# Kernel optimization log

Measured on AMD Instinct MI355X. Metric: run time of the kernel, lower is better.

Reference implementation:

```python
import jax, jax.numpy as jnp
import numpy as np

C = 128      # in channels
CO = 64      # out channels
G = 32       # group-norm groups
RES_IN = 32  # input resolution
RES_OUT = 64 # subdivided resolution
N = 20000    # active input voxels
EPS = 1e-5


def setup_inputs() -> dict:
    key = jax.random.key(0)
    ks = jax.random.split(key, 12)
    # unique active voxel coords at RES_IN (batch index 0, single instance)
    rng = np.random.default_rng(0)
    flat = rng.choice(RES_IN ** 3, size=N, replace=False)
    xyz = np.stack([flat // (RES_IN * RES_IN), (flat // RES_IN) % RES_IN, flat % RES_IN], axis=1)
    x_coords = jnp.asarray(np.concatenate([np.zeros((N, 1), np.int32), xyz.astype(np.int32)], axis=1))
    x_feats = jax.random.normal(ks[0], (N, C), dtype=jnp.float32)
    gn1_g = 1.0 + 0.1 * jax.random.normal(ks[1], (C,), dtype=jnp.float32)
    gn1_b = 0.1 * jax.random.normal(ks[2], (C,), dtype=jnp.float32)
    W1 = 0.05 * jax.random.normal(ks[3], (3, 3, 3, C, CO), dtype=jnp.float32)
    b1 = 0.01 * jax.random.normal(ks[4], (CO,), dtype=jnp.float32)
    gn2_g = 1.0 + 0.1 * jax.random.normal(ks[5], (CO,), dtype=jnp.float32)
    gn2_b = 0.1 * jax.random.normal(ks[6], (CO,), dtype=jnp.float32)
    W2 = 0.05 * jax.random.normal(ks[7], (3, 3, 3, CO, CO), dtype=jnp.float32)  # zero_module in source; random here to exercise math
    b2 = 0.01 * jax.random.normal(ks[8], (CO,), dtype=jnp.float32)
    Ws = 0.05 * jax.random.normal(ks[9], (C, CO), dtype=jnp.float32)   # 1x1 skip conv
    bs = 0.01 * jax.random.normal(ks[10], (CO,), dtype=jnp.float32)
    return dict(x_feats=x_feats, x_coords=x_coords, gn1_g=gn1_g, gn1_b=gn1_b,
                W1=W1, b1=b1, gn2_g=gn2_g, gn2_b=gn2_b, W2=W2, b2=b2, Ws=Ws, bs=bs)


def group_norm(f, g, b):
    # single-instance sparse group norm: stats per group over all points
    n, c = f.shape
    x = f.reshape(n, G, c // G)
    mu = jnp.mean(x, axis=(0, 2), keepdims=True)
    var = jnp.mean((x - mu) ** 2, axis=(0, 2), keepdims=True)
    return ((x - mu) * jax.lax.rsqrt(var + EPS)).reshape(n, c) * g + b


def subdivide(coords, feats):
    n = coords.shape[0]
    offs = jnp.stack(jnp.meshgrid(jnp.arange(2), jnp.arange(2), jnp.arange(2), indexing='ij'), -1).reshape(8, 3)
    xyz = coords[:, None, 1:] * 2 + offs[None].astype(coords.dtype)          # [n,8,3]
    bidx = jnp.broadcast_to(coords[:, None, :1], (n, 8, 1))
    new_coords = jnp.concatenate([bidx, xyz], axis=-1).reshape(n * 8, 4)
    return new_coords, jnp.repeat(feats, 8, axis=0)


def subm_conv3(coords, feats, W, b):
    # submanifold 3x3x3 sparse conv: scatter to padded dense grid, gather 27 neighbors per active site
    cin = feats.shape[1]
    grid = jnp.zeros((RES_OUT + 2, RES_OUT + 2, RES_OUT + 2, cin), feats.dtype)
    grid = grid.at[coords[:, 1] + 1, coords[:, 2] + 1, coords[:, 3] + 1].set(feats)
    acc = jnp.zeros((feats.shape[0], W.shape[-1]), feats.dtype)
    for i in range(3):
        for j in range(3):
            for k in range(3):
                nb = grid[coords[:, 1] + i, coords[:, 2] + j, coords[:, 3] + k]  # [n, cin]
                acc = acc + nb @ W[i, j, k]
    return acc + b


def reference(x_feats, x_coords, gn1_g, gn1_b, W1, b1, gn2_g, gn2_b, W2, b2, Ws, bs):
    h = jax.nn.silu(group_norm(x_feats, gn1_g, gn1_b))
    hc, hf = subdivide(x_coords, h)
    _, xf = subdivide(x_coords, x_feats)
    hf = subm_conv3(hc, hf, W1, b1)
    hf = jax.nn.silu(group_norm(hf, gn2_g, gn2_b))
    hf = subm_conv3(hc, hf, W2, b2)
    out = hf + (xf @ Ws + bs)  # residual + 1x1 skip conv (out_channels != channels)
    return out
```

## Files before the change

### kernel.cpp

```cpp
#include <hip/hip_runtime.h>
#include <hip/hip_bf16.h>
#include <math.h>

#define N_PTS 20000
#define C_IN 128
#define C_OUT 64
#define M_PTS (N_PTS*8)
#define EPS 1e-5f

typedef __attribute__((ext_vector_type(8))) short short8;
typedef __attribute__((ext_vector_type(4))) float float4v;

__device__ __forceinline__ ushort f2bf(float f){
    unsigned int i = __float_as_uint(f);
    unsigned int r = i + 0x7fffu + ((i >> 16) & 1u);
    return (ushort)(r >> 16);
}
__device__ __forceinline__ float bf2f(ushort u){ return __uint_as_float(((unsigned int)u) << 16); }
__device__ __forceinline__ float silu(float z){ return z / (1.f + expf(-z)); }
__device__ __forceinline__ int cmp5(int v){
    v &= 0x1249; v = (v | (v >> 2)) & 0x10C3; v = (v | (v >> 4)) & 0x100F; v = (v | (v >> 8)) & 0x1F;
    return v;
}


__global__ void __launch_bounds__(256) prep_kernel(
    const float* __restrict__ W1, const float* __restrict__ W2,
    ushort* __restrict__ Wt1, ushort* __restrict__ Wt2,
    int* __restrict__ pg, ushort* __restrict__ h, ushort* __restrict__ h2,
    const float* __restrict__ x, float* __restrict__ stats)
{
    const int b = blockIdx.x, tid = threadIdx.x;
    if (b < 2048){
        int idx = b * 256 + tid;
        int j = idx & 7, l = (idx >> 3) & 63, nb = (idx >> 9) & 3, kb = (idx >> 11) & 3, t = idx >> 13;
        int ci = kb * 32 + (l >> 4) * 8 + j, co = nb * 16 + (l & 15);
        int o = t >> 3, jj = t & 7;
        int ox = (o >> 2) & 1, oy = (o >> 1) & 1, oz = o & 1;
        int jx = (jj >> 2) & 1, jy = (jj >> 1) & 1, jz = jj & 1;
        float s = 0.f;
#pragma unroll
        for (int dx = -1; dx <= 1; dx++){
            if (((ox + dx) >> 1) != ox + jx - 1) continue;
#pragma unroll
            for (int dy = -1; dy <= 1; dy++){
                if (((oy + dy) >> 1) != oy + jy - 1) continue;
#pragma unroll
                for (int dz = -1; dz <= 1; dz++){
                    if (((oz + dz) >> 1) != oz + jz - 1) continue;
                    s += W1[((dx+1)*9 + (dy+1)*3 + (dz+1)) * (C_IN*64) + ci * 64 + co];
                }
            }
        }
        Wt1[idx] = f2bf(s);
    } else if (b < 2480){
        int idx = (b - 2048) * 256 + tid;
        int j = idx & 7, l = (idx >> 3) & 63, nb = (idx >> 9) & 3, kb = (idx >> 11) & 1, t = idx >> 12;
        int ci = kb * 32 + (l >> 4) * 8 + j, co = nb * 16 + (l & 15);
        Wt2[idx] = f2bf(W2[(t * C_OUT + ci) * 64 + co]);
    } else if (b < 2608){
        int i = (b - 2480) * 256 + tid;
        pg[i] = -1;
        if (b == 2480){
            if (tid < C_IN) h[(size_t)N_PTS * C_IN + tid] = 0;
            if (tid < 256){
                h2[(size_t)M_PTS * C_OUT + tid] = 0;
                h2[(size_t)M_PTS * C_OUT + 256 + tid] = 0;
            }
        }
    } else {
        __shared__ float ls[64];
        if (tid < 64) ls[tid] = 0.f;
        __syncthreads();
        const int g = tid & 31;
        const int r0 = (b - 2608) * 8 + (tid >> 5);
        float sum = 0.f, sq = 0.f;
        for (int r = r0; r < N_PTS; r += 4096){
            float4 v = *(const float4*)(x + (size_t)r * C_IN + g * 4);
            sum += v.x + v.y + v.z + v.w;
            sq  += v.x*v.x + v.y*v.y + v.z*v.z + v.w*v.w;
        }
        atomicAdd(&ls[g], sum);
        atomicAdd(&ls[32 + g], sq);
        __syncthreads();
        if (tid < 64) atomicAdd(&stats[tid], ls[tid]);
    }
}

__global__ void __launch_bounds__(256) scatter_kernel(
    const int* __restrict__ cds, int* __restrict__ pg)
{
    int i = blockIdx.x * 256 + threadIdx.x;
    if (i < N_PTS){
        const int* cd = cds + i * 4;
        pg[(cd[1] * 32 + cd[2]) * 32 + cd[3]] = i;
    }
}

__global__ void __launch_bounds__(1024) sort_kernel(
    int* __restrict__ pg, unsigned int* __restrict__ ordp)
{
    __shared__ int psum[1024];
    const int t = threadIdx.x;
    int cnt = 0;
    for (int i = 0; i < 32; i++){
        int m = t * 32 + i;
        int x = cmp5(m >> 2), y = cmp5(m >> 1), z = cmp5(m);
        cnt += (pg[(x * 32 + y) * 32 + z] >= 0) ? 1 : 0;
    }
    psum[t] = cnt;
    __syncthreads();
    for (int off = 1; off < 1024; off <<= 1){
        int v = (t >= off) ? psum[t - off] : 0;
        __syncthreads();
        psum[t] += v;
        __syncthreads();
    }
    int run = psum[t] - cnt;
    for (int i = 0; i < 32; i++){
        int m = t * 32 + i;
        int x = cmp5(m >> 2), y = cmp5(m >> 1), z = cmp5(m);
        int ci = (x * 32 + y) * 32 + z;
        int pi = pg[ci];
        if (pi >= 0){
            ordp[run] = ((unsigned int)pi << 15) | (unsigned int)((x << 10) | (y << 5) | z);
            pg[ci] = run;
            run++;
        }
    }
}

__global__ void __launch_bounds__(256) mid_kernel(
    const int* __restrict__ cds, const int* __restrict__ pg,
    const float* __restrict__ x, const float* __restrict__ stats,
    const float* __restrict__ g1, const float* __restrict__ b1, ushort* __restrict__ h,
    const float* __restrict__ Wsk, const float* __restrict__ bsk, float* __restrict__ s)
{
    __shared__ float w[C_IN * C_OUT];
    const int b = blockIdx.x, tid = threadIdx.x;
    if (b < 2500){
        int i = (b * 256 + tid) * 4;
        int row = i >> 7, c0 = i & 127;
        const int* cd = cds + row * 4;
        int rk = pg[(cd[1] * 32 + cd[2]) * 32 + cd[3]];
        int g = c0 >> 2;
        float mu = stats[g] * (1.0f / (N_PTS * 4.0f));
        float var = stats[32 + g] * (1.0f / (N_PTS * 4.0f)) - mu * mu;
        float rs = rsqrtf(var + EPS);
        float4 v = *(const float4*)(x + i);
        ushort4 o;
        o.x = f2bf(silu((v.x - mu) * rs * g1[c0+0] + b1[c0+0]));
        o.y = f2bf(silu((v.y - mu) * rs * g1[c0+1] + b1[c0+1]));
        o.z = f2bf(silu((v.z - mu) * rs * g1[c0+2] + b1[c0+2]));
        o.w = f2bf(silu((v.w - mu) * rs * g1[c0+3] + b1[c0+3]));
        *(ushort4*)(h + (size_t)rk * C_IN + c0) = o;
    } else {
        for (int j = tid; j < C_IN * C_OUT; j += 256) w[j] = Wsk[j];
        __syncthreads();
        int co = tid & 63, pr = tid >> 6;
        int p = (b - 2500) * 4 + pr;
        const int* cd = cds + p * 4;
        int rk = pg[(cd[1] * 32 + cd[2]) * 32 + cd[3]];
        const float* xr = x + (size_t)p * C_IN;
        float a = bsk[co];
        for (int cb = 0; cb < C_IN; cb += 4){
            float4 v = *(const float4*)(xr + cb);
            a += v.x * w[(cb+0)*64+co] + v.y * w[(cb+1)*64+co]
               + v.z * w[(cb+2)*64+co] + v.w * w[(cb+3)*64+co];
        }
        s[(size_t)rk * C_OUT + co] = a;
    }
}

__global__ void __launch_bounds__(256, 4) conv1_corner(
    const ushort* __restrict__ feat, const int* __restrict__ pg,
    const unsigned int* __restrict__ ordp, const ushort* __restrict__ Wt,
    const float* __restrict__ bias, ushort* __restrict__ hf1_bf,
    float* __restrict__ statsAcc)
{
    const int tid = threadIdx.x;
    const int wid = tid >> 6, l = tid & 63;
    const int r16 = l & 15, qd = l >> 4;
    const int b = blockIdx.x;
    const int tg = (b >> 6) * 8 + (b & 7);
    const int o  = (b >> 3) & 7;
    if (tg >= 79) return;
    const int tile = tg * 4 + wid;
    if (tile >= 313) return;
    const int mb = tile * 64;

    int slot = mb + l;
    int cs = slot < N_PTS ? slot : N_PTS - 1;
    int cell = (int)(ordp[cs] & 0x7FFFu);
    int px = (cell >> 10) & 31, py = (cell >> 5) & 31, pz = cell & 31;
    int ex0 = px + ((o >> 2) & 1) - 1;
    int ey0 = py + ((o >> 1) & 1) - 1;
    int ez0 = pz + (o & 1) - 1;

    int rows8[8];
#pragma unroll
    for (int j = 0; j < 8; j++){
        int cx = ex0 + ((j >> 2) & 1), cy = ey0 + ((j >> 1) & 1), cz = ez0 + (j & 1);
        int row = N_PTS;
        if ((unsigned)cx < 32u && (unsigned)cy < 32u && (unsigned)cz < 32u){
            int pi = pg[cx * 1024 + cy * 32 + cz];
            if (pi >= 0) row = pi;
        }
        rows8[j] = row;
    }

    float4v acc[16];
#pragma unroll
    for (int c = 0; c < 16; c++) acc[c] = 0.f;

#pragma unroll
    for (int j = 0; j < 8; j++){
        int fr0 = __shfl(rows8[j],      r16, 64);
        int fr1 = __shfl(rows8[j], 16 + r16, 64);
        int fr2 = __shfl(rows8[j], 32 + r16, 64);
        int fr3 = __shfl(rows8[j], 48 + r16, 64);
        const ushort* a0 = feat + (size_t)fr0 * C_IN + qd * 8;
        const ushort* a1 = feat + (size_t)fr1 * C_IN + qd * 8;
        const ushort* a2 = feat + (size_t)fr2 * C_IN + qd * 8;
        const ushort* a3 = feat + (size_t)fr3 * C_IN + qd * 8;
        const ushort* wt = Wt + (size_t)(o * 8 + j) * 8192 + l * 8;
#pragma unroll
        for (int kb = 0; kb < 4; kb++){
            short8 b0 = *(const short8*)(wt + (kb*4+0)*512);
            short8 b1 = *(const short8*)(wt + (kb*4+1)*512);
            short8 b2 = *(const short8*)(wt + (kb*4+2)*512);
            short8 b3 = *(const short8*)(wt + (kb*4+3)*512);
            short8 av0 = *(const short8*)(a0 + kb*32);
            short8 av1 = *(const short8*)(a1 + kb*32);
            short8 av2 = *(const short8*)(a2 + kb*32);
            short8 av3 = *(const short8*)(a3 + kb*32);
            acc[0]  = __builtin_amdgcn_mfma_f32_16x16x32_bf16(av0, b0, acc[0],  0, 0, 0);
            acc[1]  = __builtin_amdgcn_mfma_f32_16x16x32_bf16(av0, b1, acc[1],  0, 0, 0);
            acc[2]  = __builtin_amdgcn_mfma_f32_16x16x32_bf16(av0, b2, acc[2],  0, 0, 0);
            acc[3]  = __builtin_amdgcn_mfma_f32_16x16x32_bf16(av0, b3, acc[3],  0, 0, 0);
            acc[4]  = __builtin_amdgcn_mfma_f32_16x16x32_bf16(av1, b0, acc[4],  0, 0, 0);
            acc[5]  = __builtin_amdgcn_mfma_f32_16x16x32_bf16(av1, b1, acc[5],  0, 0, 0);
            acc[6]  = __builtin_amdgcn_mfma_f32_16x16x32_bf16(av1, b2, acc[6],  0, 0, 0);
            acc[7]  = __builtin_amdgcn_mfma_f32_16x16x32_bf16(av1, b3, acc[7],  0, 0, 0);
            acc[8]  = __builtin_amdgcn_mfma_f32_16x16x32_bf16(av2, b0, acc[8],  0, 0, 0);
            acc[9]  = __builtin_amdgcn_mfma_f32_16x16x32_bf16(av2, b1, acc[9],  0, 0, 0);
            acc[10] = __builtin_amdgcn_mfma_f32_16x16x32_bf16(av2, b2, acc[10], 0, 0, 0);
            acc[11] = __builtin_amdgcn_mfma_f32_16x16x32_bf16(av2, b3, acc[11], 0, 0, 0);
            acc[12] = __builtin_amdgcn_mfma_f32_16x16x32_bf16(av3, b0, acc[12], 0, 0, 0);
            acc[13] = __builtin_amdgcn_mfma_f32_16x16x32_bf16(av3, b1, acc[13], 0, 0, 0);
            acc[14] = __builtin_amdgcn_mfma_f32_16x16x32_bf16(av3, b2, acc[14], 0, 0, 0);
            acc[15] = __builtin_amdgcn_mfma_f32_16x16x32_bf16(av3, b3, acc[15], 0, 0, 0);
        }
    }

    float bsv[4] = { bias[r16], bias[16 + r16], bias[32 + r16], bias[48 + r16] };
    float ps[4] = {0,0,0,0}, pq[4] = {0,0,0,0};
#pragma unroll
    for (int rb = 0; rb < 4; rb++)
#pragma unroll
        for (int nb = 0; nb < 4; nb++)
#pragma unroll
            for (int rg = 0; rg < 4; rg++){
                int sl = rb * 16 + qd * 4 + rg;
                int pr = mb + sl;
                float v = acc[rb * 4 + nb][rg] + bsv[nb];
                if (pr < N_PTS){
                    hf1_bf[(size_t)(pr * 8 + o) * 64 + nb * 16 + r16] = f2bf(v);
                    ps[nb] += v; pq[nb] += v * v;
                }
            }
#pragma unroll
    for (int nb = 0; nb < 4; nb++){
        float s1 = ps[nb], s2 = pq[nb];
        s1 += __shfl_xor(s1, 16, 64); s2 += __shfl_xor(s2, 16, 64);
        s1 += __shfl_xor(s1, 32, 64); s2 += __shfl_xor(s2, 32, 64);
        if (qd == 0){
            atomicAdd(&statsAcc[64 + nb * 16 + r16], s1);
            atomicAdd(&statsAcc[128 + nb * 16 + r16], s2);
        }
    }
}

__global__ void __launch_bounds__(256, 4) conv2_corner(
    const ushort* __restrict__ feat, const int* __restrict__ pg,
    const unsigned int* __restrict__ ordp,
    const ushort* __restrict__ Wt, const float* __restrict__ bias,
    const float* __restrict__ skip, float* __restrict__ out)
{
    const int tid = threadIdx.x;
    const int wid = tid >> 6, l = tid & 63;
    const int r16 = l & 15, qd = l >> 4;
    const int b = blockIdx.x;
    const int tile = b >> 1;
    const int o = (b & 1) * 4 + wid;
    const int ox = (o >> 2) & 1, oy = (o >> 1) & 1, oz = o & 1;
    const int mb = tile * 64;

    int slot = mb + l;
    int cs = slot < N_PTS ? slot : N_PTS - 1;
    unsigned int op = ordp[cs];
    int sp = (int)(op >> 15);
    int cell = (int)(op & 0x7FFFu);
    int px = (cell >> 10) & 31, py = (cell >> 5) & 31, pz = cell & 31;
    int ex0 = px + ox - 1, ey0 = py + oy - 1, ez0 = pz + oz - 1;

    int pb[8];
#pragma unroll
    for (int j = 0; j < 8; j++){
        int cx = ex0 + ((j >> 2) & 1), cy = ey0 + ((j >> 1) & 1), cz = ez0 + (j & 1);
        int base = M_PTS;
        if ((unsigned)cx < 32u && (unsigned)cy < 32u && (unsigned)cz < 32u){
            int pi = pg[cx * 1024 + cy * 32 + cz];
            if (pi >= 0) base = pi * 8;
        }
        pb[j] = base;
    }

    float4v acc[16];
#pragma unroll
    for (int c = 0; c < 16; c++) acc[c] = 0.f;

#pragma unroll
    for (int t = 0; t < 27; t++){
        const int dx = t / 9 - 1, dy = (t / 3) % 3 - 1, dz = t % 3 - 1;
        int sx = ox + dx, sy = oy + dy, sz = oz + dz;
        int jx = (sx >> 1) - ox + 1, jy = (sy >> 1) - oy + 1, jz = (sz >> 1) - oz + 1;
        int opi = (sx & 1) * 4 + (sy & 1) * 2 + (sz & 1);
        int m00 = jz ? pb[1] : pb[0];
        int m01 = jz ? pb[3] : pb[2];
        int m10 = jz ? pb[5] : pb[4];
        int m11 = jz ? pb[7] : pb[6];
        int n0 = jy ? m01 : m00;
        int n1 = jy ? m11 : m10;
        int row = (jx ? n1 : n0) + opi;
        int fr0 = __shfl(row,      r16, 64);
        int fr1 = __shfl(row, 16 + r16, 64);
        int fr2 = __shfl(row, 32 + r16, 64);
        int fr3 = __shfl(row, 48 + r16, 64);
        const ushort* a0 = feat + (size_t)fr0 * C_OUT + qd * 8;
        const ushort* a1 = feat + (size_t)fr1 * C_OUT + qd * 8;
        const ushort* a2 = feat + (size_t)fr2 * C_OUT + qd * 8;
        const ushort* a3 = feat + (size_t)fr3 * C_OUT + qd * 8;
        const ushort* wt = Wt + (size_t)t * 4096 + l * 8;
#pragma unroll
        for (int kb = 0; kb < 2; kb++){
            short8 b0 = *(const short8*)(wt + (kb*4+0)*512);
            short8 b1 = *(const short8*)(wt + (kb*4+1)*512);
            short8 b2 = *(const short8*)(wt + (kb*4+2)*512);
            short8 b3 = *(const short8*)(wt + (kb*4+3)*512);
            short8 av0 = *(const short8*)(a0 + kb*32);
            short8 av1 = *(const short8*)(a1 + kb*32);
            short8 av2 = *(const short8*)(a2 + kb*32);
            short8 av3 = *(const short8*)(a3 + kb*32);
            acc[0]  = __builtin_amdgcn_mfma_f32_16x16x32_bf16(av0, b0, acc[0],  0, 0, 0);
            acc[1]  = __builtin_amdgcn_mfma_f32_16x16x32_bf16(av0, b1, acc[1],  0, 0, 0);
            acc[2]  = __builtin_amdgcn_mfma_f32_16x16x32_bf16(av0, b2, acc[2],  0, 0, 0);
            acc[3]  = __builtin_amdgcn_mfma_f32_16x16x32_bf16(av0, b3, acc[3],  0, 0, 0);
            acc[4]  = __builtin_amdgcn_mfma_f32_16x16x32_bf16(av1, b0, acc[4],  0, 0, 0);
            acc[5]  = __builtin_amdgcn_mfma_f32_16x16x32_bf16(av1, b1, acc[5],  0, 0, 0);
            acc[6]  = __builtin_amdgcn_mfma_f32_16x16x32_bf16(av1, b2, acc[6],  0, 0, 0);
            acc[7]  = __builtin_amdgcn_mfma_f32_16x16x32_bf16(av1, b3, acc[7],  0, 0, 0);
            acc[8]  = __builtin_amdgcn_mfma_f32_16x16x32_bf16(av2, b0, acc[8],  0, 0, 0);
            acc[9]  = __builtin_amdgcn_mfma_f32_16x16x32_bf16(av2, b1, acc[9],  0, 0, 0);
            acc[10] = __builtin_amdgcn_mfma_f32_16x16x32_bf16(av2, b2, acc[10], 0, 0, 0);
            acc[11] = __builtin_amdgcn_mfma_f32_16x16x32_bf16(av2, b3, acc[11], 0, 0, 0);
            acc[12] = __builtin_amdgcn_mfma_f32_16x16x32_bf16(av3, b0, acc[12], 0, 0, 0);
            acc[13] = __builtin_amdgcn_mfma_f32_16x16x32_bf16(av3, b1, acc[13], 0, 0, 0);
            acc[14] = __builtin_amdgcn_mfma_f32_16x16x32_bf16(av3, b2, acc[14], 0, 0, 0);
            acc[15] = __builtin_amdgcn_mfma_f32_16x16x32_bf16(av3, b3, acc[15], 0, 0, 0);
        }
    }

    float bsv[4] = { bias[r16], bias[16 + r16], bias[32 + r16], bias[48 + r16] };
#pragma unroll
    for (int rb = 0; rb < 4; rb++)
#pragma unroll
        for (int rg = 0; rg < 4; rg++){
            int sl = rb * 16 + qd * 4 + rg;
            int slt = mb + sl;
            if (slt < N_PTS){
                int spr = __shfl(sp, sl, 64);
                const float* sk = skip + (size_t)slt * 64;
#pragma unroll
                for (int nb = 0; nb < 4; nb++){
                    int co = nb * 16 + r16;
                    out[(size_t)(spr * 8 + o) * 64 + co] = acc[rb * 4 + nb][rg] + bsv[nb] + sk[co];
                }
            }
        }
}

__global__ void __launch_bounds__(256) h2_kernel(
    const ushort* __restrict__ hf1, const float* __restrict__ stats,
    const float* __restrict__ gg, const float* __restrict__ gb, ushort* __restrict__ h2)
{
    int i = (blockIdx.x * 256 + threadIdx.x) * 4;
    if (i >= M_PTS * C_OUT) return;
    int c0 = i & (C_OUT - 1);
    const float inv = 1.0f / (M_PTS * 2.0f);
    float muA = (stats[64 + c0] + stats[64 + c0 + 1]) * inv;
    float vA  = (stats[128 + c0] + stats[128 + c0 + 1]) * inv - muA * muA;
    float rsA = rsqrtf(vA + EPS);
    float muB = (stats[64 + c0 + 2] + stats[64 + c0 + 3]) * inv;
    float vB  = (stats[128 + c0 + 2] + stats[128 + c0 + 3]) * inv - muB * muB;
    float rsB = rsqrtf(vB + EPS);
    ushort4 u = *(const ushort4*)(hf1 + i);
    ushort4 o;
    o.x = f2bf(silu((bf2f(u.x) - muA) * rsA * gg[c0+0] + gb[c0+0]));
    o.y = f2bf(silu((bf2f(u.y) - muA) * rsA * gg[c0+1] + gb[c0+1]));
    o.z = f2bf(silu((bf2f(u.z) - muB) * rsB * gg[c0+2] + gb[c0+2]));
    o.w = f2bf(silu((bf2f(u.w) - muB) * rsB * gg[c0+3] + gb[c0+3]));
    *(ushort4*)(h2 + i) = o;
}

extern "C" void kernel_launch(void* const* d_in, const int* in_sizes, int n_in,
                              void* d_out, int out_size, void* d_ws, size_t ws_size,
                              hipStream_t stream){
    const float* x   = (const float*)d_in[0];
    const int*   cds = (const int*)  d_in[1];
    const float* g1  = (const float*)d_in[2];
    const float* b1  = (const float*)d_in[3];
    const float* W1  = (const float*)d_in[4];
    const float* bb1 = (const float*)d_in[5];
    const float* g2  = (const float*)d_in[6];
    const float* b2  = (const float*)d_in[7];
    const float* W2  = (const float*)d_in[8];
    const float* bb2 = (const float*)d_in[9];
    const float* Wsk = (const float*)d_in[10];
    const float* bsk = (const float*)d_in[11];
    float* out = (float*)d_out;
    char* ws = (char*)d_ws;

    float*  stats = (float*) (ws);
    int*    pg    = (int*)   (ws + 1024);
    ushort* h     = (ushort*)(ws + 132096);
    ushort* h2    = (ushort*)(ws + 5252352);
    float*  s     = (float*) (ws + 25733376);
    ushort* Wt1   = (ushort*)(ws + 30853376);
    ushort* Wt2   = (ushort*)(ws + 31901952);
    unsigned int* ordp = (unsigned int*)(ws + 32123136);

    hipMemsetAsync(stats, 0, 192 * sizeof(float), stream);
    prep_kernel<<<3120, 256, 0, stream>>>(W1, W2, Wt1, Wt2, pg, h, h2, x, stats);
    scatter_kernel<<<79, 256, 0, stream>>>(cds, pg);
    sort_kernel<<<1, 1024, 0, stream>>>(pg, ordp);
    mid_kernel<<<7500, 256, 0, stream>>>(cds, pg, x, stats, g1, b1, h, Wsk, bsk, s);
    conv1_corner<<<640, 256, 0, stream>>>(h, pg, ordp, Wt1, bb1, (ushort*)d_out, stats);
    h2_kernel<<<12500, 256, 0, stream>>>((const ushort*)d_out, stats, g2, b2, h2);
    conv2_corner<<<626, 256, 0, stream>>>(h2, pg, ordp, Wt2, bb2, s, out);
}
```

Before: 402.0 us.

## Split sort into parallel kernels, XCD-aware tiling, double-buffer conv2 loads, coalesce output

The single-block sort is split into three kernels: a parallel count over 16 blocks, a one-block prefix scan, and a parallel placement pass. This spreads the serial gather work across more compute units. conv1 and conv2 now map block IDs so that neighbouring tiles land on the same XCD, which should improve L2 reuse. conv2 precomputes its 27 neighbour rows and double-buffers the A-fragment loads so the next tap's gathers overlap the current MFMAs. It also stages outputs in a 64KB shared buffer so each point's 4 corner outputs are written as contiguous float4 rows. The price is higher register and LDS pressure, which lowers occupancy from 4 blocks per CU to 2.

Measured after the change: 375.0 us. 6.7% less time.

```diff
diff --git a/kernel.cpp b/kernel.cpp
--- a/kernel.cpp
+++ b/kernel.cpp
@@ -97,26 +97,40 @@
     }
 }
 
-__global__ void __launch_bounds__(1024) sort_kernel(
-    int* __restrict__ pg, unsigned int* __restrict__ ordp)
-{
-    __shared__ int psum[1024];
-    const int t = threadIdx.x;
-    int cnt = 0;
+__global__ void __launch_bounds__(64) sortA_kernel(
+    const int* __restrict__ pg, int* __restrict__ cnt)
+{
+    int t = blockIdx.x * 64 + threadIdx.x;
+    int c = 0;
     for (int i = 0; i < 32; i++){
         int m = t * 32 + i;
         int x = cmp5(m >> 2), y = cmp5(m >> 1), z = cmp5(m);
-        cnt += (pg[(x * 32 + y) * 32 + z] >= 0) ? 1 : 0;
-    }
-    psum[t] = cnt;
+        c += (pg[(x * 32 + y) * 32 + z] >= 0) ? 1 : 0;
+    }
+    cnt[t] = c;
+}
+__global__ void __launch_bounds__(1024) sortB_kernel(
+    const int* __restrict__ cnt, int* __restrict__ base)
+{
+    __shared__ int ps[1024];
+    const int t = threadIdx.x;
+    int c = cnt[t];
+    ps[t] = c;
     __syncthreads();
     for (int off = 1; off < 1024; off <<= 1){
-        int v = (t >= off) ? psum[t - off] : 0;
+        int v = (t >= off) ? ps[t - off] : 0;
         __syncthreads();
-        psum[t] += v;
+        ps[t] += v;
         __syncthreads();
     }
-    int run = psum[t] - cnt;
+    base[t] = ps[t] - c;
+}
+__global__ void __launch_bounds__(64) sortC_kernel(
+    int* __restrict__ pg, unsigned int* __restrict__ ordp,
+    const int* __restrict__ base)
+{
+    int t = blockIdx.x * 64 + threadIdx.x;
+    int run = base[t];
     for (int i = 0; i < 32; i++){
         int m = t * 32 + i;
         int x = cmp5(m >> 2), y = cmp5(m >> 1), z = cmp5(m);
@@ -182,9 +196,9 @@
     const int wid = tid >> 6, l = tid & 63;
     const int r16 = l & 15, qd = l >> 4;
     const int b = blockIdx.x;
-    const int tg = (b >> 6) * 8 + (b & 7);
-    const int o  = (b >> 3) & 7;
-    if (tg >= 79) return;
+    const int xcd = b & 7, k = b >> 3;
+    const int tg = xcd * 10 + (k >> 3);
+    const int o  = k & 7;
     const int tile = tg * 4 + wid;
     if (tile >= 313) return;
     const int mb = tile * 64;
@@ -281,25 +295,30 @@
     }
 }
 
-__global__ void __launch_bounds__(256, 4) conv2_corner(
+__global__ void __launch_bounds__(256, 2) conv2_corner(
     const ushort* __restrict__ feat, const int* __restrict__ pg,
     const unsigned int* __restrict__ ordp,
     const ushort* __restrict__ Wt, const float* __restrict__ bias,
     const float* __restrict__ skip, float* __restrict__ out)
 {
+    __shared__ float lout[64][4][64];
+    __shared__ int sprs[64];
     const int tid = threadIdx.x;
     const int wid = tid >> 6, l = tid & 63;
     const int r16 = l & 15, qd = l >> 4;
     const int b = blockIdx.x;
-    const int tile = b >> 1;
-    const int o = (b & 1) * 4 + wid;
+    const int xcd = b & 7, k = b >> 3;
+    const int tile = xcd * 40 + (k >> 1);
+    const int half = k & 1;
+    if (tile >= 313) return;
+    const int o = half * 4 + wid;
     const int ox = (o >> 2) & 1, oy = (o >> 1) & 1, oz = o & 1;
     const int mb = tile * 64;
 
     int slot = mb + l;
     int cs = slot < N_PTS ? slot : N_PTS - 1;
     unsigned int op = ordp[cs];
-    int sp = (int)(op >> 15);
+    if (wid == 0) sprs[l] = (int)(op >> 15);
     int cell = (int)(op & 0x7FFFu);
     int px = (cell >> 10) & 31, py = (cell >> 5) & 31, pz = cell & 31;
     int ex0 = px + ox - 1, ey0 = py + oy - 1, ez0 = pz + oz - 1;
@@ -316,10 +335,7 @@
         pb[j] = base;
     }
 
-    float4v acc[16];
-#pragma unroll
-    for (int c = 0; c < 16; c++) acc[c] = 0.f;
-
+    int rowT[27];
 #pragma unroll
     for (int t = 0; t < 27; t++){
         const int dx = t / 9 - 1, dy = (t / 3) % 3 - 1, dz = t % 3 - 1;
@@ -332,7 +348,15 @@
         int m11 = jz ? pb[7] : pb[6];
         int n0 = jy ? m01 : m00;
         int n1 = jy ? m11 : m10;
-        int row = (jx ? n1 : n0) + opi;
+        rowT[t] = (jx ? n1 : n0) + opi;
+    }
+
+    float4v acc[16];
+#pragma unroll
+    for (int c = 0; c < 16; c++) acc[c] = 0.f;
+
+    auto loadA = [&](int t, short8* av){
+        int row = rowT[t];
         int fr0 = __shfl(row,      r16, 64);
         int fr1 = __shfl(row, 16 + r16, 64);
         int fr2 = __shfl(row, 32 + r16, 64);
@@ -341,6 +365,19 @@
         const ushort* a1 = feat + (size_t)fr1 * C_OUT + qd * 8;
         const ushort* a2 = feat + (size_t)fr2 * C_OUT + qd * 8;
         const ushort* a3 = feat + (size_t)fr3 * C_OUT + qd * 8;
+        av[0] = *(const short8*)(a0);      av[1] = *(const short8*)(a0 + 32);
+        av[2] = *(const short8*)(a1);      av[3] = *(const short8*)(a1 + 32);
+        av[4] = *(const short8*)(a2);      av[5] = *(const short8*)(a2 + 32);
+        av[6] = *(const short8*)(a3);      av[7] = *(const short8*)(a3 + 32);
+    };
+
+    short8 avA[8], avB[8];
+    loadA(0, avA);
+#pragma unroll
+    for (int t = 0; t < 27; t++){
+        short8* cur = (t & 1) ? avB : avA;
+        short8* nxt = (t & 1) ? avA : avB;
+        if (t + 1 < 27) loadA(t + 1, nxt);
         const ushort* wt = Wt + (size_t)t * 4096 + l * 8;
 #pragma unroll
         for (int kb = 0; kb < 2; kb++){
@@ -348,26 +385,22 @@
             short8 b1 = *(const short8*)(wt + (kb*4+1)*512);
             short8 b2 = *(const short8*)(wt + (kb*4+2)*512);
             short8 b3 = *(const short8*)(wt + (kb*4+3)*512);
-            short8 av0 = *(const short8*)(a0 + kb*32);
-            short8 av1 = *(const short8*)(a1 + kb*32);
-            short8 av2 = *(const short8*)(a2 + kb*32);
-            short8 av3 = *(const short8*)(a3 + kb*32);
-            acc[0]  = __builtin_amdgcn_mfma_f32_16x16x32_bf16(av0, b0, acc[0],  0, 0, 0);
-            acc[1]  = __builtin_amdgcn_mfma_f32_16x16x32_bf16(av0, b1, acc[1],  0, 0, 0);
-            acc[2]  = __builtin_amdgcn_mfma_f32_16x16x32_bf16(av0, b2, acc[2],  0, 0, 0);
-            acc[3]  = __builtin_amdgcn_mfma_f32_16x16x32_bf16(av0, b3, acc[3],  0, 0, 0);
-            acc[4]  = __builtin_amdgcn_mfma_f32_16x16x32_bf16(av1, b0, acc[4],  0, 0, 0);
-            acc[5]  = __builtin_amdgcn_mfma_f32_16x16x32_bf16(av1, b1, acc[5],  0, 0, 0);
-            acc[6]  = __builtin_amdgcn_mfma_f32_16x16x32_bf16(av1, b2, acc[6],  0, 0, 0);
-            acc[7]  = __builtin_amdgcn_mfma_f32_16x16x32_bf16(av1, b3, acc[7],  0, 0, 0);
-            acc[8]  = __builtin_amdgcn_mfma_f32_16x16x32_bf16(av2, b0, acc[8],  0, 0, 0);
-            acc[9]  = __builtin_amdgcn_mfma_f32_16x16x32_bf16(av2, b1, acc[9],  0, 0, 0);
-            acc[10] = __builtin_amdgcn_mfma_f32_16x16x32_bf16(av2, b2, acc[10], 0, 0, 0);
-            acc[11] = __builtin_amdgcn_mfma_f32_16x16x32_bf16(av2, b3, acc[11], 0, 0, 0);
-            acc[12] = __builtin_amdgcn_mfma_f32_16x16x32_bf16(av3, b0, acc[12], 0, 0, 0);
-            acc[13] = __builtin_amdgcn_mfma_f32_16x16x32_bf16(av3, b1, acc[13], 0, 0, 0);
-            acc[14] = __builtin_amdgcn_mfma_f32_16x16x32_bf16(av3, b2, acc[14], 0, 0, 0);
-            acc[15] = __builtin_amdgcn_mfma_f32_16x16x32_bf16(av3, b3, acc[15], 0, 0, 0);
+            acc[0]  = __builtin_amdgcn_mfma_f32_16x16x32_bf16(cur[0*2+kb], b0, acc[0],  0, 0, 0);
+            acc[1]  = __builtin_amdgcn_mfma_f32_16x16x32_bf16(cur[0*2+kb], b1, acc[1],  0, 0, 0);
+            acc[2]  = __builtin_amdgcn_mfma_f32_16x16x32_bf16(cur[0*2+kb], b2, acc[2],  0, 0, 0);
+            acc[3]  = __builtin_amdgcn_mfma_f32_16x16x32_bf16(cur[0*2+kb], b3, acc[3],  0, 0, 0);
+            acc[4]  = __builtin_amdgcn_mfma_f32_16x16x32_bf16(cur[1*2+kb], b0, acc[4],  0, 0, 0);
+            acc[5]  = __builtin_amdgcn_mfma_f32_16x16x32_bf16(cur[1*2+kb], b1, acc[5],  0, 0, 0);
+            acc[6]  = __builtin_amdgcn_mfma_f32_16x16x32_bf16(cur[1*2+kb], b2, acc[6],  0, 0, 0);
+            acc[7]  = __builtin_amdgcn_mfma_f32_16x16x32_bf16(cur[1*2+kb], b3, acc[7],  0, 0, 0);
+            acc[8]  = __builtin_amdgcn_mfma_f32_16x16x32_bf16(cur[2*2+kb], b0, acc[8],  0, 0, 0);
+            acc[9]  = __builtin_amdgcn_mfma_f32_16x16x32_bf16(cur[2*2+kb], b1, acc[9],  0, 0, 0);
+            acc[10] = __builtin_amdgcn_mfma_f32_16x16x32_bf16(cur[2*2+kb], b2, acc[10], 0, 0, 0);
+            acc[11] = __builtin_amdgcn_mfma_f32_16x16x32_bf16(cur[2*2+kb], b3, acc[11], 0, 0, 0);
+            acc[12] = __builtin_amdgcn_mfma_f32_16x16x32_bf16(cur[3*2+kb], b0, acc[12], 0, 0, 0);
+            acc[13] = __builtin_amdgcn_mfma_f32_16x16x32_bf16(cur[3*2+kb], b1, acc[13], 0, 0, 0);
+            acc[14] = __builtin_amdgcn_mfma_f32_16x16x32_bf16(cur[3*2+kb], b2, acc[14], 0, 0, 0);
+            acc[15] = __builtin_amdgcn_mfma_f32_16x16x32_bf16(cur[3*2+kb], b3, acc[15], 0, 0, 0);
         }
     }
 
@@ -377,17 +410,22 @@
 #pragma unroll
         for (int rg = 0; rg < 4; rg++){
             int sl = rb * 16 + qd * 4 + rg;
-            int slt = mb + sl;
-            if (slt < N_PTS){
-                int spr = __shfl(sp, sl, 64);
-                const float* sk = skip + (size_t)slt * 64;
-#pragma unroll
-                for (int nb = 0; nb < 4; nb++){
-                    int co = nb * 16 + r16;
-                    out[(size_t)(spr * 8 + o) * 64 + co] = acc[rb * 4 + nb][rg] + bsv[nb] + sk[co];
-                }
-            }
-        }
+            int slc = (mb + sl < N_PTS) ? (mb + sl) : (N_PTS - 1);
+            const float* sk = skip + (size_t)slc * 64;
+#pragma unroll
+            for (int nb = 0; nb < 4; nb++)
+                lout[sl][wid][nb * 16 + r16] = acc[rb * 4 + nb][rg] + bsv[nb] + sk[nb * 16 + r16];
+        }
+    __syncthreads();
+#pragma unroll
+    for (int r = 0; r < 16; r++){
+        int idx = r * 1024 + tid * 4;
+        int s = idx >> 8, off = idx & 255;
+        if (mb + s < N_PTS){
+            float4 v = *(const float4*)&lout[s][0][off];
+            *(float4*)(out + ((size_t)sprs[s] * 8 + half * 4) * 64 + off) = v;
+        }
+    }
 }
 
 __global__ void __launch_bounds__(256) h2_kernel(
@@ -439,13 +477,17 @@
     ushort* Wt1   = (ushort*)(ws + 30853376);
     ushort* Wt2   = (ushort*)(ws + 31901952);
     unsigned int* ordp = (unsigned int*)(ws + 32123136);
+    int*    cnt   = (int*)   (ws + 32203136);
+    int*    base  = (int*)   (ws + 32207232);
 
     hipMemsetAsync(stats, 0, 192 * sizeof(float), stream);
     prep_kernel<<<3120, 256, 0, stream>>>(W1, W2, Wt1, Wt2, pg, h, h2, x, stats);
     scatter_kernel<<<79, 256, 0, stream>>>(cds, pg);
-    sort_kernel<<<1, 1024, 0, stream>>>(pg, ordp);
+    sortA_kernel<<<16, 64, 0, stream>>>(pg, cnt);
+    sortB_kernel<<<1, 1024, 0, stream>>>(cnt, base);
+    sortC_kernel<<<16, 64, 0, stream>>>(pg, ordp, base);
     mid_kernel<<<7500, 256, 0, stream>>>(cds, pg, x, stats, g1, b1, h, Wsk, bsk, s);
     conv1_corner<<<640, 256, 0, stream>>>(h, pg, ordp, Wt1, bb1, (ushort*)d_out, stats);
     h2_kernel<<<12500, 256, 0, stream>>>((const ushort*)d_out, stats, g2, b2, h2);
-    conv2_corner<<<626, 256, 0, stream>>>(h2, pg, ordp, Wt2, bb2, s, out);
-}
+    conv2_corner<<<640, 256, 0, stream>>>(h2, pg, ordp, Wt2, bb2, s, out);
+}
```
